# Performance work log

Hardware: AMD Instinct MI355X
Metric: run time of the kernel (lower is better)

The kernel has to match this reference:

```python
import jax, jax.numpy as jnp
import numpy as np

N, E = 50000, 800000
IN, OUT, HEADS = 128, 128, 4
HID = OUT // HEADS  # 32
NEG_SLOPE = 0.2  # PyG GATv2Conv default


def setup_inputs() -> dict:
    key = jax.random.key(0)
    ks = jax.random.split(key, 12)
    s = 0.05
    return {
        "x": jax.random.normal(ks[0], (N, IN), jnp.float32),
        "edge_index": jax.random.randint(ks[1], (2, E), 0, N, jnp.int64),
        "edge_weight": jax.random.uniform(ks[2], (E,), jnp.float32),
        "h": jax.random.normal(ks[3], (N, OUT), jnp.float32),
        "Wl": jax.random.normal(ks[4], (IN, HEADS * HID), jnp.float32) * s,
        "Wr": jax.random.normal(ks[5], (IN, HEADS * HID), jnp.float32) * s,
        "att": jax.random.normal(ks[6], (HEADS, HID), jnp.float32) * s,
        "bias_conv": jnp.zeros((HEADS * HID,), jnp.float32),
        "W1": jax.random.normal(ks[7], (2 * OUT, 2 * OUT), jnp.float32) * s,
        "b1": jnp.zeros((2 * OUT,), jnp.float32),
        "W2": jax.random.normal(ks[8], (2 * OUT, OUT), jnp.float32) * s,
        "b2": jnp.zeros((OUT,), jnp.float32),
    }


def gatv2_conv(x, edge_index, Wl, Wr, att, bias_conv):
    n = x.shape[0]
    heads, hid = att.shape
    # add self loops (PyG default add_self_loops=True)
    loops = jnp.arange(n, dtype=edge_index.dtype)
    src = jnp.concatenate([edge_index[0], loops])
    dst = jnp.concatenate([edge_index[1], loops])
    xl = (x @ Wl).reshape(n, heads, hid)  # source transform
    xr = (x @ Wr).reshape(n, heads, hid)  # target transform
    m = xl[src] + xr[dst]                  # [E+N, H, D]
    e = jnp.einsum('ehd,hd->eh', jax.nn.leaky_relu(m, NEG_SLOPE), att)
    mx = jax.ops.segment_max(e, dst, num_segments=n)
    a = jnp.exp(e - mx[dst])
    denom = jax.ops.segment_sum(a, dst, num_segments=n)
    alpha = a / (denom[dst] + 1e-16)       # segment softmax over in-edges
    out = jax.ops.segment_sum(xl[src] * alpha[..., None], dst, num_segments=n)
    return out.reshape(n, heads * hid) + bias_conv


def reference(x, edge_index, edge_weight, h, Wl, Wr, att, bias_conv, W1, b1, W2, b2):
    # edge_weight is accepted by TGATCell.forward but never used
    f = jax.nn.sigmoid(gatv2_conv(x, edge_index, Wl, Wr, att, bias_conv))
    ru = jax.nn.sigmoid(jnp.concatenate([f, h], axis=1) @ W1 + b1)
    r, u = jnp.split(ru, 2, axis=1)
    c = jnp.tanh(jnp.concatenate([f, r * h], axis=1) @ W2 + b2)
    return u * h + (1.0 - u) * c
```

## Files before the change

### kernel.cpp

```cpp
#include <hip/hip_runtime.h>
#include <hip/hip_bf16.h>
#include <math.h>

typedef __attribute__((ext_vector_type(8))) short short8;
typedef __attribute__((ext_vector_type(4))) float floatx4;

__device__ __forceinline__ unsigned short f2b(float f) {
  unsigned int u = __builtin_bit_cast(unsigned int, f);
  u += 0x7fffu + ((u >> 16) & 1u);
  return (unsigned short)(u >> 16);
}
__device__ __forceinline__ float b2f(unsigned short s) {
  unsigned int u = ((unsigned int)s) << 16;
  return __builtin_bit_cast(float, u);
}
__device__ __forceinline__ float blo(unsigned int u) {
  return __builtin_bit_cast(float, u << 16);
}
__device__ __forceinline__ float bhi(unsigned int u) {
  return __builtin_bit_cast(float, u & 0xffff0000u);
}
__device__ __forceinline__ float sigm(float v) { return 1.f / (1.f + __expf(-v)); }
__device__ __forceinline__ float tanh_fast(float y) {
  float t = __expf(2.f * y);
  return 1.f - 2.f / (t + 1.f);
}

__device__ __forceinline__ int probe_flag(const void* ei, int E) {
  __shared__ int fl;
  if (threadIdx.x == 0) fl = 0;
  __syncthreads();
  if (threadIdx.x < 64) {
    long long pos = (long long)threadIdx.x * (E / 64) + (E / 128);
    if (pos >= E) pos = E - 1;
    unsigned int v = ((const unsigned int*)ei)[2 * pos + 1];
    if (v != 0u) atomicOr(&fl, 1);
  }
  __syncthreads();
  return fl;
}

__device__ __forceinline__ int load_dst(const void* ei, int E, int flag, int i) {
  if (flag == 0) return (int)((const long long*)ei)[(long long)E + i];
  return ((const int*)ei)[E + i];
}
__device__ __forceinline__ int load_src(const void* ei, int E, int flag, int i) {
  if (flag == 0) return (int)((const long long*)ei)[i];
  return ((const int*)ei)[i];
}

__global__ __launch_bounds__(256) void bucket_hist(const void* __restrict__ ei, int E,
                                                   int* __restrict__ bucketCnt, int nbk) {
  __shared__ int h[512];
  int fl = probe_flag(ei, E);
  for (int i = threadIdx.x; i < nbk; i += 256) h[i] = 0;
  __syncthreads();
  int gid = blockIdx.x * 256 + threadIdx.x;
  int stride = gridDim.x * 256;
  for (int i = gid; i < E; i += stride) {
    int d = load_dst(ei, E, fl, i);
    atomicAdd(&h[d >> 7], 1);
  }
  __syncthreads();
  for (int i = threadIdx.x; i < nbk; i += 256)
    if (h[i]) atomicAdd(&bucketCnt[i], h[i]);
}

__global__ __launch_bounds__(64) void bucket_scan(const int* __restrict__ bucketCnt,
                                                  int* __restrict__ bucketBase,
                                                  int* __restrict__ bucketCursor, int nbk) {
  int lane = threadIdx.x;
  int carry = 0;
  for (int base = 0; base < nbk; base += 64) {
    int i = base + lane;
    int v = (i < nbk) ? bucketCnt[i] : 0;
    int s = v;
    #pragma unroll
    for (int ofs = 1; ofs < 64; ofs <<= 1) {
      int t = __shfl_up(s, ofs, 64);
      if (lane >= ofs) s += t;
    }
    if (i < nbk) {
      int ex = s - v + carry;
      bucketBase[i] = ex;
      bucketCursor[i] = ex;
    }
    carry += __shfl(s, 63, 64);
  }
  if (lane == 0) bucketBase[nbk] = carry;
}

__global__ __launch_bounds__(256) void partition_kernel(const void* __restrict__ ei, int E,
                                                        int* __restrict__ bucketCursor,
                                                        unsigned long long* __restrict__ pairBuf,
                                                        int nbk) {
  __shared__ int h[512];
  __shared__ int base[512];
  int fl = probe_flag(ei, E);
  int tid = threadIdx.x;
  for (int i = tid; i < nbk; i += 256) h[i] = 0;
  __syncthreads();
  int tile0 = blockIdx.x * 4096;
  int sarr[16], darr[16], rank[16];
  #pragma unroll
  for (int k = 0; k < 16; ++k) {
    int idx = tile0 + tid + k * 256;
    rank[k] = -1;
    if (idx < E) {
      sarr[k] = load_src(ei, E, fl, idx);
      darr[k] = load_dst(ei, E, fl, idx);
      rank[k] = atomicAdd(&h[darr[k] >> 7], 1);
    }
  }
  __syncthreads();
  for (int i = tid; i < nbk; i += 256)
    base[i] = h[i] ? atomicAdd(&bucketCursor[i], h[i]) : 0;
  __syncthreads();
  #pragma unroll
  for (int k = 0; k < 16; ++k) {
    if (rank[k] >= 0) {
      int bk = darr[k] >> 7;
      pairBuf[(size_t)base[bk] + rank[k]] =
          ((unsigned long long)(unsigned)darr[k] << 32) | (unsigned)sarr[k];
    }
  }
}

__global__ __launch_bounds__(256) void csr_build(const unsigned long long* __restrict__ pairBuf,
                                                 const int* __restrict__ bucketBase,
                                                 int* __restrict__ off, int* __restrict__ csr,
                                                 int n, int E, int nbk) {
  __shared__ int cnt[128];
  __shared__ int start[128];
  __shared__ int wtot[4];
  int bk = blockIdx.x;
  int tid = threadIdx.x;
  int lo = bucketBase[bk], hi = bucketBase[bk + 1];
  int node0 = bk << 7;
  if (tid < 128) cnt[tid] = 0;
  __syncthreads();
  for (int i = lo + tid; i < hi; i += 256) {
    int d = (int)(pairBuf[i] >> 32);
    atomicAdd(&cnt[d - node0], 1);
  }
  __syncthreads();
  {
    int v = (tid < 128) ? cnt[tid] : 0;
    int s = v;
    #pragma unroll
    for (int ofs = 1; ofs < 64; ofs <<= 1) {
      int t = __shfl_up(s, ofs, 64);
      if ((tid & 63) >= ofs) s += t;
    }
    if ((tid & 63) == 63) wtot[tid >> 6] = s;
    __syncthreads();
    if (tid < 128) {
      int pre = (tid >> 6) ? wtot[0] : 0;
      start[tid] = s - v + pre;
    }
  }
  __syncthreads();
  int nNodes = n - node0;
  if (nNodes > 128) nNodes = 128;
  if (tid < nNodes) off[node0 + tid] = lo + start[tid];
  if (bk == nbk - 1 && tid == 0) off[n] = E;
  if (tid < 128) cnt[tid] = 0;
  __syncthreads();
  for (int i = lo + tid; i < hi; i += 256) {
    unsigned long long pr = pairBuf[i];
    int s = (int)(unsigned)pr;
    int ld = (int)(pr >> 32) - node0;
    int r = atomicAdd(&cnt[ld], 1);
    csr[lo + start[ld] + r] = s;
  }
}

__global__ __launch_bounds__(256) void wprep(const float* __restrict__ Wl,
                                             const float* __restrict__ Wr,
                                             const float* __restrict__ W1,
                                             const float* __restrict__ W2,
                                             unsigned short* __restrict__ Btfxw,
                                             unsigned short* __restrict__ Btf1,
                                             unsigned short* __restrict__ Btf2) {
  int gid = blockIdx.x * 256 + threadIdx.x;
  if (gid < 4096) {
    int lane = gid & 63, fid = gid >> 6;
    int l15 = lane & 15, lhi = lane >> 4;
    int kk = fid & 3, nt = (fid >> 2) & 3, w = fid >> 4;
    int col = w * 64 + nt * 16 + l15;
    int k0 = kk * 32 + lhi * 8;
    #pragma unroll
    for (int e = 0; e < 8; ++e) {
      float v = (col < 128) ? Wl[(k0 + e) * 128 + col] : Wr[(k0 + e) * 128 + (col - 128)];
      Btfxw[(size_t)gid * 8 + e] = f2b(v);
    }
  } else if (gid < 12288) {
    int g = gid - 4096;
    int lane = g & 63, fid = g >> 6;
    int l15 = lane & 15, lhi = lane >> 4;
    int kk = fid & 1, ks = (fid >> 1) & 3, nt = (fid >> 3) & 3, w = fid >> 5;
    int col = (nt < 2) ? (w * 32 + nt * 16 + l15) : (128 + w * 32 + (nt - 2) * 16 + l15);
    int k0 = ks * 64 + kk * 32 + lhi * 8;
    #pragma unroll
    for (int e = 0; e < 8; ++e)
      Btf1[(size_t)g * 8 + e] = f2b(W1[(k0 + e) * 256 + col]);
  } else {
    int g = gid - 12288;
    int lane = g & 63, fid = g >> 6;
    int l15 = lane & 15, lhi = lane >> 4;
    int kk = fid & 1, ks = (fid >> 1) & 3, nt = (fid >> 3) & 1, w = fid >> 4;
    int col = w * 32 + nt * 16 + l15;
    int k0 = ks * 64 + kk * 32 + lhi * 8;
    #pragma unroll
    for (int e = 0; e < 8; ++e)
      Btf2[(size_t)g * 8 + e] = f2b(W2[(k0 + e) * 128 + col]);
  }
}

__global__ __launch_bounds__(256) void gemm_xw(const float* __restrict__ x,
                                               const unsigned short* __restrict__ Btf,
                                               unsigned short* __restrict__ xl,
                                               unsigned short* __restrict__ xr, int n) {
  __shared__ char As[32 * 256];
  int t = threadIdx.x;
  int w = t >> 6, l = t & 63;
  int row0 = blockIdx.x * 32;
  int l15 = l & 15, lhi = l >> 4;

  #pragma unroll
  for (int u_ = 0; u_ < 2; ++u_) {
    int unit = t + u_ * 256;
    int r = unit >> 4, slot = unit & 15;
    int grow = row0 + r;
    uint4 o = make_uint4(0, 0, 0, 0);
    if (grow < n) {
      const float* s = x + (size_t)grow * 128 + slot * 8;
      float4 f0 = *(const float4*)s, f1 = *(const float4*)(s + 4);
      o.x = (unsigned)f2b(f0.x) | ((unsigned)f2b(f0.y) << 16);
      o.y = (unsigned)f2b(f0.z) | ((unsigned)f2b(f0.w) << 16);
      o.z = (unsigned)f2b(f1.x) | ((unsigned)f2b(f1.y) << 16);
      o.w = (unsigned)f2b(f1.z) | ((unsigned)f2b(f1.w) << 16);
    }
    *(uint4*)(As + r * 256 + ((slot * 16) ^ ((r & 7) << 4))) = o;
  }
  __syncthreads();

  floatx4 acc[2][4];
  #pragma unroll
  for (int mt = 0; mt < 2; ++mt)
    #pragma unroll
    for (int nt = 0; nt < 4; ++nt) acc[mt][nt] = (floatx4){0.f, 0.f, 0.f, 0.f};

  short8 bcur[4], bnext[4];
  #pragma unroll
  for (int nt = 0; nt < 4; ++nt)
    bcur[nt] = *(const short8*)(Btf + (((size_t)(w * 4 + nt) * 4 + 0) * 64 + l) * 8);

  #pragma unroll 1
  for (int kk = 0; kk < 4; ++kk) {
    if (kk < 3) {
      #pragma unroll
      for (int nt = 0; nt < 4; ++nt)
        bnext[nt] = *(const short8*)(Btf + (((size_t)(w * 4 + nt) * 4 + kk + 1) * 64 + l) * 8);
    }
    int ko = kk * 64 + lhi * 16;
    short8 a[2];
    #pragma unroll
    for (int mt = 0; mt < 2; ++mt) {
      int r = mt * 16 + l15;
      a[mt] = *(const short8*)(As + r * 256 + (ko ^ ((r & 7) << 4)));
    }
    #pragma unroll
    for (int nt = 0; nt < 4; ++nt)
      #pragma unroll
      for (int mt = 0; mt < 2; ++mt)
        acc[mt][nt] = __builtin_amdgcn_mfma_f32_16x16x32_bf16(a[mt], bcur[nt], acc[mt][nt], 0, 0, 0);
    if (kk < 3) {
      #pragma unroll
      for (int nt = 0; nt < 4; ++nt) bcur[nt] = bnext[nt];
    }
  }

  #pragma unroll
  for (int mt = 0; mt < 2; ++mt)
    #pragma unroll
    for (int nt = 0; nt < 4; ++nt) {
      int col = w * 64 + nt * 16 + l15;
      int rbase = row0 + mt * 16 + lhi * 4;
      #pragma unroll
      for (int j = 0; j < 4; ++j) {
        int row = rbase + j;
        if (row >= n) continue;
        unsigned short v = f2b(acc[mt][nt][j]);
        if (col < 128) xl[(size_t)row * 128 + col] = v;
        else           xr[(size_t)row * 128 + (col - 128)] = v;
      }
    }
}

__global__ __launch_bounds__(256) void node_kernel(const unsigned int* __restrict__ xl32,
                                                   const unsigned int* __restrict__ xr32,
                                                   const float* __restrict__ att,
                                                   const float* __restrict__ bias,
                                                   const int* __restrict__ off,
                                                   const int* __restrict__ csr,
                                                   unsigned int* __restrict__ fout, int n) {
  int wid = threadIdx.x >> 6, lane = threadIdx.x & 63;
  int node = blockIdx.x * 4 + wid;
  if (node >= n) return;
  int hl = lane & 31;
  bool upper = lane >= 32;
  const float LOG2E = 1.44269504f;
  float4 av = *(const float4*)(att + hl * 4);
  float a0 = av.x * LOG2E, a1 = av.y * LOG2E, a2 = av.z * LOG2E, a3 = av.w * LOG2E;
  uint2 xrp = *(const uint2*)(xr32 + node * 64 + hl * 2);
  float xr0 = blo(xrp.x), xr1 = bhi(xrp.x);
  float xr2 = blo(xrp.y), xr3 = bhi(xrp.y);
  float num0 = 0.f, num1 = 0.f, num2 = 0.f, num3 = 0.f, den = 0.f;
  int beg = off[node], end = off[node + 1];

  auto edge2 = [&](int sLo, int sHi, bool hiValid) {
    int s = upper ? sHi : sLo;
    uint2 g = *(const uint2*)(xl32 + ((unsigned)s << 6) + (unsigned)(hl << 1));
    float x0 = blo(g.x), x1 = bhi(g.x), x2 = blo(g.y), x3 = bhi(g.y);
    float m0 = x0 + xr0, m1 = x1 + xr1, m2 = x2 + xr2, m3 = x3 + xr3;
    float l0 = fmaxf(m0, 0.2f * m0), l1 = fmaxf(m1, 0.2f * m1);
    float l2 = fmaxf(m2, 0.2f * m2), l3 = fmaxf(m3, 0.2f * m3);
    float p = l0 * a0;
    p = fmaf(l1, a1, p);
    p = fmaf(l2, a2, p);
    p = fmaf(l3, a3, p);
    p += __shfl_xor(p, 1, 64);
    p += __shfl_xor(p, 2, 64);
    p += __shfl_xor(p, 4, 64);
    float wgt = __builtin_amdgcn_exp2f(p);
    if (upper && !hiValid) wgt = 0.f;
    num0 = fmaf(wgt, x0, num0);
    num1 = fmaf(wgt, x1, num1);
    num2 = fmaf(wgt, x2, num2);
    num3 = fmaf(wgt, x3, num3);
    den += wgt;
  };

  if (beg < end) {
    edge2(node, csr[beg], true);
    for (int base = beg + 1; base < end; base += 64) {
      int cnt = end - base;
      if (cnt > 64) cnt = 64;
      int my = csr[base + (lane < cnt ? lane : 0)];
      int i = 0;
      for (; i + 4 <= cnt; i += 4) {
        int sa = __builtin_amdgcn_readlane(my, i);
        int sb = __builtin_amdgcn_readlane(my, i + 1);
        int sc = __builtin_amdgcn_readlane(my, i + 2);
        int sd = __builtin_amdgcn_readlane(my, i + 3);
        edge2(sa, sb, true);
        edge2(sc, sd, true);
      }
      for (; i + 2 <= cnt; i += 2) {
        int sa = __builtin_amdgcn_readlane(my, i);
        int sb = __builtin_amdgcn_readlane(my, i + 1);
        edge2(sa, sb, true);
      }
      if (i < cnt) edge2(__builtin_amdgcn_readlane(my, i), node, false);
    }
  } else {
    edge2(node, node, false);
  }

  num0 += __shfl_xor(num0, 32, 64);
  num1 += __shfl_xor(num1, 32, 64);
  num2 += __shfl_xor(num2, 32, 64);
  num3 += __shfl_xor(num3, 32, 64);
  den  += __shfl_xor(den, 32, 64);

  if (!upper) {
    float inv = 1.f / (den + 1e-16f);
    float4 bv = *(const float4*)(bias + hl * 4);
    float v0 = num0 * inv + bv.x;
    float v1 = num1 * inv + bv.y;
    float v2 = num2 * inv + bv.z;
    float v3 = num3 * inv + bv.w;
    uint2 o;
    o.x = (unsigned)f2b(sigm(v0)) | ((unsigned)f2b(sigm(v1)) << 16);
    o.y = (unsigned)f2b(sigm(v2)) | ((unsigned)f2b(sigm(v3)) << 16);
    *(uint2*)(fout + node * 64 + hl * 2) = o;
  }
}

__global__ __launch_bounds__(256) void gemm_fused(const unsigned short* __restrict__ fbuf,
                                                  const float* __restrict__ hf,
                                                  const unsigned short* __restrict__ Btf1,
                                                  const unsigned short* __restrict__ Btf2,
                                                  const float* __restrict__ b1,
                                                  const float* __restrict__ b2,
                                                  float* __restrict__ out, int n) {
  __shared__ char As[32 * 512];
  int t = threadIdx.x;
  int w = t >> 6, l = t & 63;
  int row0 = blockIdx.x * 32;
  int l15 = l & 15, lhi = l >> 4;

  #pragma unroll
  for (int u_ = 0; u_ < 4; ++u_) {
    int unit = t + u_ * 256;
    int r = unit >> 5, slot = unit & 31;
    int koff = slot * 16;
    int grow = row0 + r;
    uint4 v = make_uint4(0, 0, 0, 0);
    if (grow < n) {
      if (koff < 256) {
        v = *(const uint4*)(fbuf + (size_t)grow * 128 + koff / 2);
      } else {
        const float* s = hf + (size_t)grow * 128 + (koff - 256) / 2;
        float4 f0 = *(const float4*)s, f1 = *(const float4*)(s + 4);
        v.x = (unsigned)f2b(f0.x) | ((unsigned)f2b(f0.y) << 16);
        v.y = (unsigned)f2b(f0.z) | ((unsigned)f2b(f0.w) << 16);
        v.z = (unsigned)f2b(f1.x) | ((unsigned)f2b(f1.y) << 16);
        v.w = (unsigned)f2b(f1.z) | ((unsigned)f2b(f1.w) << 16);
      }
    }
    *(uint4*)(As + r * 512 + (koff ^ ((r & 7) << 4))) = v;
  }
  __syncthreads();

  floatx4 acc[2][4];
  #pragma unroll
  for (int mt = 0; mt < 2; ++mt)
    #pragma unroll
    for (int nt = 0; nt < 4; ++nt) acc[mt][nt] = (floatx4){0.f, 0.f, 0.f, 0.f};

  short8 bcur[4], bnext[4];
  #pragma unroll
  for (int nt = 0; nt < 4; ++nt)
    bcur[nt] = *(const short8*)(Btf1 + (((size_t)(w * 4 + nt) * 8 + 0) * 64 + l) * 8);

  #pragma unroll 1
  for (int step = 0; step < 8; ++step) {
    if (step < 7) {
      #pragma unroll
      for (int nt = 0; nt < 4; ++nt)
        bnext[nt] = *(const short8*)(Btf1 + (((size_t)(w * 4 + nt) * 8 + step + 1) * 64 + l) * 8);
    }
    int ka = step * 64 + lhi * 16;
    short8 a[2];
    #pragma unroll
    for (int mt = 0; mt < 2; ++mt) {
      int r = mt * 16 + l15;
      a[mt] = *(const short8*)(As + r * 512 + (ka ^ ((r & 7) << 4)));
    }
    #pragma unroll
    for (int nt = 0; nt < 4; ++nt)
      #pragma unroll
      for (int mt = 0; mt < 2; ++mt)
        acc[mt][nt] = __builtin_amdgcn_mfma_f32_16x16x32_bf16(a[mt], bcur[nt], acc[mt][nt], 0, 0, 0);
    if (step < 7) {
      #pragma unroll
      for (int nt = 0; nt < 4; ++nt) bcur[nt] = bnext[nt];
    }
  }
  __syncthreads();

  float us[2][2][4];
  #pragma unroll
  for (int mt = 0; mt < 2; ++mt)
    #pragma unroll
    for (int nt = 0; nt < 4; ++nt) {
      #pragma unroll
      for (int j = 0; j < 4; ++j) {
        int rloc = mt * 16 + lhi * 4 + j;
        if (nt < 2) {
          int col = w * 32 + nt * 16 + l15;
          float s = sigm(acc[mt][nt][j] + b1[col]);
          int byteoff = (256 + col * 2) ^ ((rloc & 7) << 4);
          char* p = As + rloc * 512 + byteoff;
          unsigned short hv = *(unsigned short*)p;
          *(unsigned short*)p = f2b(s * b2f(hv));
        } else {
          int col = 128 + w * 32 + (nt - 2) * 16 + l15;
          us[mt][nt - 2][j] = sigm(acc[mt][nt][j] + b1[col]);
        }
      }
    }
  __syncthreads();

  floatx4 acc2[2][2];
  #pragma unroll
  for (int mt = 0; mt < 2; ++mt)
    #pragma unroll
    for (int nt = 0; nt < 2; ++nt) acc2[mt][nt] = (floatx4){0.f, 0.f, 0.f, 0.f};

  short8 bcur2[2], bnext2[2];
  #pragma unroll
  for (int nt = 0; nt < 2; ++nt)
    bcur2[nt] = *(const short8*)(Btf2 + (((size_t)(w * 2 + nt) * 8 + 0) * 64 + l) * 8);

  #pragma unroll 1
  for (int step = 0; step < 8; ++step) {
    if (step < 7) {
      #pragma unroll
      for (int nt = 0; nt < 2; ++nt)
        bnext2[nt] = *(const short8*)(Btf2 + (((size_t)(w * 2 + nt) * 8 + step + 1) * 64 + l) * 8);
    }
    int ka = step * 64 + lhi * 16;
    short8 a[2];
    #pragma unroll
    for (int mt = 0; mt < 2; ++mt) {
      int r = mt * 16 + l15;
      a[mt] = *(const short8*)(As + r * 512 + (ka ^ ((r & 7) << 4)));
    }
    #pragma unroll
    for (int nt = 0; nt < 2; ++nt)
      #pragma unroll
      for (int mt = 0; mt < 2; ++mt)
        acc2[mt][nt] = __builtin_amdgcn_mfma_f32_16x16x32_bf16(a[mt], bcur2[nt], acc2[mt][nt], 0, 0, 0);
    if (step < 7) {
      #pragma unroll
      for (int nt = 0; nt < 2; ++nt) bcur2[nt] = bnext2[nt];
    }
  }

  #pragma unroll
  for (int mt = 0; mt < 2; ++mt)
    #pragma unroll
    for (int nt = 0; nt < 2; ++nt) {
      int col = w * 32 + nt * 16 + l15;
      #pragma unroll
      for (int j = 0; j < 4; ++j) {
        int rloc = mt * 16 + lhi * 4 + j;
        int row = row0 + rloc;
        if (row >= n) continue;
        float c = tanh_fast(acc2[mt][nt][j] + b2[col]);
        float uu = us[mt][nt][j];
        float hv = hf[(size_t)row * 128 + col];
        out[(size_t)row * 128 + col] = uu * hv + (1.f - uu) * c;
      }
    }
}

extern "C" void kernel_launch(void* const* d_in, const int* in_sizes, int n_in,
                              void* d_out, int out_size, void* d_ws, size_t ws_size,
                              hipStream_t stream) {
  const float* x     = (const float*)d_in[0];
  const void*  ei    = d_in[1];
  const float* h     = (const float*)d_in[3];
  const float* Wl    = (const float*)d_in[4];
  const float* Wr    = (const float*)d_in[5];
  const float* att   = (const float*)d_in[6];
  const float* bconv = (const float*)d_in[7];
  const float* W1    = (const float*)d_in[8];
  const float* b1    = (const float*)d_in[9];
  const float* W2    = (const float*)d_in[10];
  const float* b2    = (const float*)d_in[11];
  float* out = (float*)d_out;

  const int n = in_sizes[0] / 128;
  const int E = in_sizes[1] / 2;
  const int nbk = (n + 127) >> 7;

  char* w = (char*)d_ws;
  size_t o = 0;
  auto alloc = [&](size_t bytes) {
    char* p = w + o;
    o += bytes;
    o = (o + 255) & ~(size_t)255;
    return p;
  };
  int* bucketCnt    = (int*)alloc((size_t)nbk * 4);
  int* bucketBase   = (int*)alloc((size_t)(nbk + 1) * 4);
  int* bucketCursor = (int*)alloc((size_t)nbk * 4);
  int* off          = (int*)alloc((size_t)(n + 1) * 4);
  int* csr          = (int*)alloc((size_t)E * 4);
  unsigned long long* pairBuf = (unsigned long long*)alloc((size_t)E * 8);
  unsigned short* xl   = (unsigned short*)alloc((size_t)n * 128 * 2);
  unsigned short* xr   = (unsigned short*)alloc((size_t)n * 128 * 2);
  unsigned short* fbuf = (unsigned short*)alloc((size_t)n * 128 * 2);
  unsigned short* Btfxw = (unsigned short*)alloc(4096 * 8 * 2);
  unsigned short* Btf1  = (unsigned short*)alloc(8192 * 8 * 2);
  unsigned short* Btf2  = (unsigned short*)alloc(4096 * 8 * 2);

  hipMemsetAsync(bucketCnt, 0, (size_t)nbk * 4, stream);
  bucket_hist<<<256, 256, 0, stream>>>(ei, E, bucketCnt, nbk);
  bucket_scan<<<1, 64, 0, stream>>>(bucketCnt, bucketBase, bucketCursor, nbk);
  partition_kernel<<<(E + 4095) / 4096, 256, 0, stream>>>(ei, E, bucketCursor, pairBuf, nbk);
  csr_build<<<nbk, 256, 0, stream>>>(pairBuf, bucketBase, off, csr, n, E, nbk);
  wprep<<<64, 256, 0, stream>>>(Wl, Wr, W1, W2, Btfxw, Btf1, Btf2);

  int gblocks = (n + 31) / 32;
  gemm_xw<<<gblocks, 256, 0, stream>>>(x, Btfxw, xl, xr, n);
  node_kernel<<<(n + 3) / 4, 256, 0, stream>>>((const unsigned int*)xl, (const unsigned int*)xr,
                                               att, bconv, off, csr,
                                               (unsigned int*)fbuf, n);
  gemm_fused<<<gblocks, 256, 0, stream>>>(fbuf, h, Btf1, Btf2, b1, b2, out, n);
}
```

Measured before the change: 146.4 us.

## Merge independent prep kernels into combined launches via block-range dispatch

Merges the weight-repacking kernel into the bucket histogram kernel, using extra blocks beyond 256, and merges the CSR build with the x@W GEMM into one launch split by block index. This cuts two kernel launches and lets the independent CSR build and projection GEMM run concurrently on the GPU instead of back to back. The trade-off is higher shared-memory use per block for the CSR blocks, since they now also reserve the GEMM tile buffer, and the GEMM's Btfxw dependency now relies on prep1 finishing earlier in the stream.

Measured after the change: 136.0 us. 1.08x faster.

```diff
diff --git a/kernel.cpp b/kernel.cpp
--- a/kernel.cpp
+++ b/kernel.cpp
@@ -49,21 +49,64 @@
   return ((const int*)ei)[i];
 }
 
-__global__ __launch_bounds__(256) void bucket_hist(const void* __restrict__ ei, int E,
-                                                   int* __restrict__ bucketCnt, int nbk) {
+__global__ __launch_bounds__(256) void prep1(const void* __restrict__ ei, int E,
+                                             int* __restrict__ bucketCnt, int nbk,
+                                             const float* __restrict__ Wl,
+                                             const float* __restrict__ Wr,
+                                             const float* __restrict__ W1,
+                                             const float* __restrict__ W2,
+                                             unsigned short* __restrict__ Btfxw,
+                                             unsigned short* __restrict__ Btf1,
+                                             unsigned short* __restrict__ Btf2) {
   __shared__ int h[512];
-  int fl = probe_flag(ei, E);
-  for (int i = threadIdx.x; i < nbk; i += 256) h[i] = 0;
-  __syncthreads();
-  int gid = blockIdx.x * 256 + threadIdx.x;
-  int stride = gridDim.x * 256;
-  for (int i = gid; i < E; i += stride) {
-    int d = load_dst(ei, E, fl, i);
-    atomicAdd(&h[d >> 7], 1);
-  }
-  __syncthreads();
-  for (int i = threadIdx.x; i < nbk; i += 256)
-    if (h[i]) atomicAdd(&bucketCnt[i], h[i]);
+  if (blockIdx.x < 256) {
+    int fl = probe_flag(ei, E);
+    for (int i = threadIdx.x; i < nbk; i += 256) h[i] = 0;
+    __syncthreads();
+    int gid = blockIdx.x * 256 + threadIdx.x;
+    int stride = 256 * 256;
+    for (int i = gid; i < E; i += stride) {
+      int d = load_dst(ei, E, fl, i);
+      atomicAdd(&h[d >> 7], 1);
+    }
+    __syncthreads();
+    for (int i = threadIdx.x; i < nbk; i += 256)
+      if (h[i]) atomicAdd(&bucketCnt[i], h[i]);
+  } else {
+    int gid = (blockIdx.x - 256) * 256 + threadIdx.x;
+    if (gid < 4096) {
+      int lane = gid & 63, fid = gid >> 6;
+      int l15 = lane & 15, lhi = lane >> 4;
+      int kk = fid & 3, nt = (fid >> 2) & 3, w = fid >> 4;
+      int col = w * 64 + nt * 16 + l15;
+      int k0 = kk * 32 + lhi * 8;
+      #pragma unroll
+      for (int e = 0; e < 8; ++e) {
+        float v = (col < 128) ? Wl[(k0 + e) * 128 + col] : Wr[(k0 + e) * 128 + (col - 128)];
+        Btfxw[(size_t)gid * 8 + e] = f2b(v);
+      }
+    } else if (gid < 12288) {
+      int g = gid - 4096;
+      int lane = g & 63, fid = g >> 6;
+      int l15 = lane & 15, lhi = lane >> 4;
+      int kk = fid & 1, ks = (fid >> 1) & 3, nt = (fid >> 3) & 3, w = fid >> 5;
+      int col = (nt < 2) ? (w * 32 + nt * 16 + l15) : (128 + w * 32 + (nt - 2) * 16 + l15);
+      int k0 = ks * 64 + kk * 32 + lhi * 8;
+      #pragma unroll
+      for (int e = 0; e < 8; ++e)
+        Btf1[(size_t)g * 8 + e] = f2b(W1[(k0 + e) * 256 + col]);
+    } else {
+      int g = gid - 12288;
+      int lane = g & 63, fid = g >> 6;
+      int l15 = lane & 15, lhi = lane >> 4;
+      int kk = fid & 1, ks = (fid >> 1) & 3, nt = (fid >> 3) & 1, w = fid >> 4;
+      int col = w * 32 + nt * 16 + l15;
+      int k0 = ks * 64 + kk * 32 + lhi * 8;
+      #pragma unroll
+      for (int e = 0; e < 8; ++e)
+        Btf2[(size_t)g * 8 + e] = f2b(W2[(k0 + e) * 128 + col]);
+    }
+  }
 }
 
 __global__ __launch_bounds__(64) void bucket_scan(const int* __restrict__ bucketCnt,
@@ -126,110 +169,71 @@
   }
 }
 
-__global__ __launch_bounds__(256) void csr_build(const unsigned long long* __restrict__ pairBuf,
-                                                 const int* __restrict__ bucketBase,
-                                                 int* __restrict__ off, int* __restrict__ csr,
-                                                 int n, int E, int nbk) {
+__global__ __launch_bounds__(256) void csr_xw(const unsigned long long* __restrict__ pairBuf,
+                                              const int* __restrict__ bucketBase,
+                                              int* __restrict__ off, int* __restrict__ csr,
+                                              int n, int E, int nbk,
+                                              const float* __restrict__ x,
+                                              const unsigned short* __restrict__ Btf,
+                                              unsigned short* __restrict__ xl,
+                                              unsigned short* __restrict__ xr) {
+  __shared__ char As[32 * 256];
   __shared__ int cnt[128];
   __shared__ int start[128];
   __shared__ int wtot[4];
-  int bk = blockIdx.x;
   int tid = threadIdx.x;
-  int lo = bucketBase[bk], hi = bucketBase[bk + 1];
-  int node0 = bk << 7;
-  if (tid < 128) cnt[tid] = 0;
-  __syncthreads();
-  for (int i = lo + tid; i < hi; i += 256) {
-    int d = (int)(pairBuf[i] >> 32);
-    atomicAdd(&cnt[d - node0], 1);
-  }
-  __syncthreads();
-  {
-    int v = (tid < 128) ? cnt[tid] : 0;
-    int s = v;
-    #pragma unroll
-    for (int ofs = 1; ofs < 64; ofs <<= 1) {
-      int t = __shfl_up(s, ofs, 64);
-      if ((tid & 63) >= ofs) s += t;
-    }
-    if ((tid & 63) == 63) wtot[tid >> 6] = s;
+
+  if (blockIdx.x < (unsigned)nbk) {
+    int bk = blockIdx.x;
+    int lo = bucketBase[bk], hi = bucketBase[bk + 1];
+    int node0 = bk << 7;
+    if (tid < 128) cnt[tid] = 0;
     __syncthreads();
-    if (tid < 128) {
-      int pre = (tid >> 6) ? wtot[0] : 0;
-      start[tid] = s - v + pre;
-    }
-  }
-  __syncthreads();
-  int nNodes = n - node0;
-  if (nNodes > 128) nNodes = 128;
-  if (tid < nNodes) off[node0 + tid] = lo + start[tid];
-  if (bk == nbk - 1 && tid == 0) off[n] = E;
-  if (tid < 128) cnt[tid] = 0;
-  __syncthreads();
-  for (int i = lo + tid; i < hi; i += 256) {
-    unsigned long long pr = pairBuf[i];
-    int s = (int)(unsigned)pr;
-    int ld = (int)(pr >> 32) - node0;
-    int r = atomicAdd(&cnt[ld], 1);
-    csr[lo + start[ld] + r] = s;
-  }
-}
-
-__global__ __launch_bounds__(256) void wprep(const float* __restrict__ Wl,
-                                             const float* __restrict__ Wr,
-                                             const float* __restrict__ W1,
-                                             const float* __restrict__ W2,
-                                             unsigned short* __restrict__ Btfxw,
-                                             unsigned short* __restrict__ Btf1,
-                                             unsigned short* __restrict__ Btf2) {
-  int gid = blockIdx.x * 256 + threadIdx.x;
-  if (gid < 4096) {
-    int lane = gid & 63, fid = gid >> 6;
-    int l15 = lane & 15, lhi = lane >> 4;
-    int kk = fid & 3, nt = (fid >> 2) & 3, w = fid >> 4;
-    int col = w * 64 + nt * 16 + l15;
-    int k0 = kk * 32 + lhi * 8;
-    #pragma unroll
-    for (int e = 0; e < 8; ++e) {
-      float v = (col < 128) ? Wl[(k0 + e) * 128 + col] : Wr[(k0 + e) * 128 + (col - 128)];
-      Btfxw[(size_t)gid * 8 + e] = f2b(v);
-    }
-  } else if (gid < 12288) {
-    int g = gid - 4096;
-    int lane = g & 63, fid = g >> 6;
-    int l15 = lane & 15, lhi = lane >> 4;
-    int kk = fid & 1, ks = (fid >> 1) & 3, nt = (fid >> 3) & 3, w = fid >> 5;
-    int col = (nt < 2) ? (w * 32 + nt * 16 + l15) : (128 + w * 32 + (nt - 2) * 16 + l15);
-    int k0 = ks * 64 + kk * 32 + lhi * 8;
-    #pragma unroll
-    for (int e = 0; e < 8; ++e)
-      Btf1[(size_t)g * 8 + e] = f2b(W1[(k0 + e) * 256 + col]);
-  } else {
-    int g = gid - 12288;
-    int lane = g & 63, fid = g >> 6;
-    int l15 = lane & 15, lhi = lane >> 4;
-    int kk = fid & 1, ks = (fid >> 1) & 3, nt = (fid >> 3) & 1, w = fid >> 4;
-    int col = w * 32 + nt * 16 + l15;
-    int k0 = ks * 64 + kk * 32 + lhi * 8;
-    #pragma unroll
-    for (int e = 0; e < 8; ++e)
-      Btf2[(size_t)g * 8 + e] = f2b(W2[(k0 + e) * 128 + col]);
-  }
-}
-
-__global__ __launch_bounds__(256) void gemm_xw(const float* __restrict__ x,
-                                               const unsigned short* __restrict__ Btf,
-                                               unsigned short* __restrict__ xl,
-                                               unsigned short* __restrict__ xr, int n) {
-  __shared__ char As[32 * 256];
-  int t = threadIdx.x;
-  int w = t >> 6, l = t & 63;
-  int row0 = blockIdx.x * 32;
+    for (int i = lo + tid; i < hi; i += 256) {
+      int d = (int)(pairBuf[i] >> 32);
+      atomicAdd(&cnt[d - node0], 1);
+    }
+    __syncthreads();
+    {
+      int v = (tid < 128) ? cnt[tid] : 0;
+      int s = v;
+      #pragma unroll
+      for (int ofs = 1; ofs < 64; ofs <<= 1) {
+        int t = __shfl_up(s, ofs, 64);
+        if ((tid & 63) >= ofs) s += t;
+      }
+      if ((tid & 63) == 63) wtot[tid >> 6] = s;
+      __syncthreads();
+      if (tid < 128) {
+        int pre = (tid >> 6) ? wtot[0] : 0;
+        start[tid] = s - v + pre;
+      }
+    }
+    __syncthreads();
+    int nNodes = n - node0;
+    if (nNodes > 128) nNodes = 128;
+    if (tid < nNodes) off[node0 + tid] = lo + start[tid];
+    if (bk == nbk - 1 && tid == 0) off[n] = E;
+    if (tid < 128) cnt[tid] = 0;
+    __syncthreads();
+    for (int i = lo + tid; i < hi; i += 256) {
+      unsigned long long pr = pairBuf[i];
+      int s = (int)(unsigned)pr;
+      int ld = (int)(pr >> 32) - node0;
+      int r = atomicAdd(&cnt[ld], 1);
+      csr[lo + start[ld] + r] = s;
+    }
+    return;
+  }
+
+  int bid = blockIdx.x - nbk;
+  int w = tid >> 6, l = tid & 63;
+  int row0 = bid * 32;
   int l15 = l & 15, lhi = l >> 4;
 
   #pragma unroll
   for (int u_ = 0; u_ < 2; ++u_) {
-    int unit = t + u_ * 256;
+    int unit = tid + u_ * 256;
     int r = unit >> 4, slot = unit & 15;
     int grow = row0 + r;
     uint4 o = make_uint4(0, 0, 0, 0);
@@ -579,15 +583,14 @@
   unsigned short* Btf1  = (unsigned short*)alloc(8192 * 8 * 2);
   unsigned short* Btf2  = (unsigned short*)alloc(4096 * 8 * 2);
 
+  int gblocks = (n + 31) / 32;
+
   hipMemsetAsync(bucketCnt, 0, (size_t)nbk * 4, stream);
-  bucket_hist<<<256, 256, 0, stream>>>(ei, E, bucketCnt, nbk);
+  prep1<<<320, 256, 0, stream>>>(ei, E, bucketCnt, nbk, Wl, Wr, W1, W2, Btfxw, Btf1, Btf2);
   bucket_scan<<<1, 64, 0, stream>>>(bucketCnt, bucketBase, bucketCursor, nbk);
   partition_kernel<<<(E + 4095) / 4096, 256, 0, stream>>>(ei, E, bucketCursor, pairBuf, nbk);
-  csr_build<<<nbk, 256, 0, stream>>>(pairBuf, bucketBase, off, csr, n, E, nbk);
-  wprep<<<64, 256, 0, stream>>>(Wl, Wr, W1, W2, Btfxw, Btf1, Btf2);
-
-  int gblocks = (n + 31) / 32;
-  gemm_xw<<<gblocks, 256, 0, stream>>>(x, Btfxw, xl, xr, n);
+  csr_xw<<<nbk + gblocks, 256, 0, stream>>>(pairBuf, bucketBase, off, csr, n, E, nbk,
+                                            x, Btfxw, xl, xr);
   node_kernel<<<(n + 3) / 4, 256, 0, stream>>>((const unsigned int*)xl, (const unsigned int*)xr,
                                                att, bconv, off, csr,
                                                (unsigned int*)fbuf, n);
```
